# Kernel tuning notes

Hardware: AMD Instinct MI355X
Metric: run time of the kernel (lower is better)

## Reference

```python
import jax, jax.numpy as jnp
import numpy as np

K = 32          # neighbors_for_lrf
EPS = 1e-12     # safe-sqrt epsilon (self-distance is exactly 0)


def shot_lrf(neighborhoods, radii):
    """SHOT local reference frames.
    neighborhoods: (N, K, 3) neighbor offsets (neighbor - center)
    radii:         (N,) support radius (distance to farthest of the K neighbors)
    returns        (N, 3, 3) rows = [x, y, z] axes
    """
    k = neighborhoods.shape[1]
    dists = jnp.sqrt(jnp.maximum(jnp.sum(neighborhoods ** 2, axis=-1), EPS))  # (N,K)
    w = radii[:, None] - dists                                                # (N,K) SHOT weights
    cov = jnp.einsum("nk,nki,nkj->nij", w, neighborhoods, neighborhoods)
    cov = cov / jnp.sum(w, axis=-1)[:, None, None]                            # (N,3,3)

    _, evecs = jnp.linalg.eigh(cov)            # ascending eigenvalues
    x = evecs[:, :, 2]                          # largest-eigenvalue eigenvector
    z = evecs[:, :, 0]                          # smallest-eigenvalue eigenvector

    # Sign disambiguation: orient axis toward the majority of neighbors.
    px = jnp.einsum("nki,ni->nk", neighborhoods, x)
    n_pos_x = jnp.sum(px >= 0, axis=-1)
    x = jnp.where((n_pos_x >= k - n_pos_x)[:, None], x, -x)

    pz = jnp.einsum("nki,ni->nk", neighborhoods, z)
    n_pos_z = jnp.sum(pz >= 0, axis=-1)
    z = jnp.where((n_pos_z >= k - n_pos_z)[:, None], z, -z)

    y = jnp.cross(z, x)
    return jnp.stack([x, y, z], axis=1)         # (N,3,3)


def knn_shot_lrf(k, verts):
    """verts: (N,3) -> (N,3,3) LRFs via KNN + weighted-covariance eigendecomposition."""
    d2 = jnp.sum((verts[:, None, :] - verts[None, :, :]) ** 2, axis=-1)  # (N,N)
    dist = jnp.sqrt(jnp.maximum(d2, EPS))
    neg_top, idx = jax.lax.top_k(-dist, k)      # k nearest (includes self)
    radii = -neg_top[:, -1]                     # distance to farthest kept neighbor
    nbh = verts[idx] - verts[:, None, :]        # (N,K,3) gathered, centered neighborhoods
    return shot_lrf(nbh, radii)


def setup_inputs() -> dict:
    key = jax.random.key(0)
    vertices = jax.random.normal(key, (2, 8192, 3), dtype=jnp.float32)
    return {"vertices": vertices}


def reference(vertices):
    B, N = vertices.shape[0], vertices.shape[1]
    lrfs = jax.vmap(lambda v: knn_shot_lrf(K, v))(vertices)  # (B,N,3,3)
    return lrfs.reshape(B, N, 9)
```

## Files before the change

kernel.cpp:

```cpp
#include <hip/hip_runtime.h>
#include <stdint.h>

#define NPTS 8192
#define KNN  32
#define WAVES 8
#define BTHR (WAVES*64)
#define CAP  512
#define K2BLK 64

#define G     16
#define NCELL 4096
#define TOTC  8192
#define NB    (TOTC/1024)
#define GLO   (-6.0f)
#define GINV  (1.3333334f)

#define EPSF    5.9604645e-08f
#define EPS2F   3.5527137e-15f
#define SAFMINF 1.17549435e-38f
#define SAFMAXF 8.5070592e+37f
#define RTMINF  1.0842022e-19f
#define RTMAXF  9.2233720e+18f

__device__ __forceinline__ float fsignf(float a, float b) {
  return __builtin_copysignf(fabsf(a), b);
}

__device__ __forceinline__ float slapy2f(float x, float y) {
  float xa = fabsf(x), ya = fabsf(y);
  float w = fmaxf(xa, ya), z = fminf(xa, ya);
  if (z == 0.0f) return w;
  float t = __fdiv_rn(z, w);
  return __fmul_rn(w, __fsqrt_rn(__fadd_rn(1.0f, __fmul_rn(t, t))));
}

__device__ __forceinline__ void slartgf(float f, float g, float& c, float& s, float& r) {
  if (g == 0.0f)      { c = 1.0f; s = 0.0f; r = f; }
  else if (f == 0.0f) { c = 0.0f; s = __builtin_copysignf(1.0f, g); r = fabsf(g); }
  else {
    float f1 = fabsf(f), g1 = fabsf(g);
    if (f1 > RTMINF && f1 < RTMAXF && g1 > RTMINF && g1 < RTMAXF) {
      float d = __fsqrt_rn(__fadd_rn(__fmul_rn(f, f), __fmul_rn(g, g)));
      c = __fdiv_rn(f1, d);
      r = __builtin_copysignf(d, f);
      s = __fdiv_rn(g, r);
    } else {
      float u  = fminf(SAFMAXF, fmaxf(SAFMINF, fmaxf(f1, g1)));
      float fs = __fdiv_rn(f, u), gs = __fdiv_rn(g, u);
      float d  = __fsqrt_rn(__fadd_rn(__fmul_rn(fs, fs), __fmul_rn(gs, gs)));
      c = __fdiv_rn(fabsf(fs), d);
      r = __builtin_copysignf(d, f);
      s = __fdiv_rn(gs, r);
      r = __fmul_rn(r, u);
    }
  }
}

__device__ void slaev2f(float a, float b, float c,
                        float& rt1, float& rt2, float& cs1, float& sn1) {
  float sm = __fadd_rn(a, c), df = __fsub_rn(a, c);
  float adf = fabsf(df), tb = __fadd_rn(b, b), ab = fabsf(tb);
  float acmx, acmn;
  if (fabsf(a) > fabsf(c)) { acmx = a; acmn = c; } else { acmx = c; acmn = a; }
  float rt;
  if (adf > ab) {
    float t = __fdiv_rn(ab, adf);
    rt = __fmul_rn(adf, __fsqrt_rn(__fadd_rn(1.0f, __fmul_rn(t, t))));
  } else if (adf < ab) {
    float t = __fdiv_rn(adf, ab);
    rt = __fmul_rn(ab, __fsqrt_rn(__fadd_rn(1.0f, __fmul_rn(t, t))));
  } else {
    rt = __fmul_rn(ab, __fsqrt_rn(2.0f));
  }
  int sgn1;
  if (sm < 0.0f) {
    rt1 = __fmul_rn(0.5f, __fsub_rn(sm, rt)); sgn1 = -1;
    rt2 = __fsub_rn(__fmul_rn(__fdiv_rn(acmx, rt1), acmn), __fmul_rn(__fdiv_rn(b, rt1), b));
  } else if (sm > 0.0f) {
    rt1 = __fmul_rn(0.5f, __fadd_rn(sm, rt)); sgn1 = 1;
    rt2 = __fsub_rn(__fmul_rn(__fdiv_rn(acmx, rt1), acmn), __fmul_rn(__fdiv_rn(b, rt1), b));
  } else {
    rt1 = __fmul_rn(0.5f, rt); rt2 = -rt1; sgn1 = 1;
  }
  float cs; int sgn2;
  if (df >= 0.0f) { cs = __fadd_rn(df, rt); sgn2 = 1; }
  else            { cs = __fsub_rn(df, rt); sgn2 = -1; }
  float acs = fabsf(cs);
  if (acs > ab) {
    float ct = __fdiv_rn(-tb, cs);
    sn1 = __fdiv_rn(1.0f, __fsqrt_rn(__fadd_rn(1.0f, __fmul_rn(ct, ct))));
    cs1 = __fmul_rn(ct, sn1);
  } else {
    if (ab == 0.0f) { cs1 = 1.0f; sn1 = 0.0f; }
    else {
      float tn = __fdiv_rn(-cs, tb);
      cs1 = __fdiv_rn(1.0f, __fsqrt_rn(__fadd_rn(1.0f, __fmul_rn(tn, tn))));
      sn1 = __fmul_rn(tn, cs1);
    }
  }
  if (sgn1 == sgn2) { float tn = cs1; cs1 = -sn1; sn1 = tn; }
}

#define ZZ(i,j) base[((i)*3+(j))*K2BLK]
#define DD(i)   base[(9+(i))*K2BLK]
#define EE(i)   base[(12+(i))*K2BLK]
#define CW(i)   base[(14+(i))*K2BLK]
#define SW(i)   base[(16+(i))*K2BLK]

__device__ void steqr3f(float* base) {
  const int nmaxit = 90;
  int jtot = 0;
  int l1 = 0;
  for (int outer = 0; outer < 6; ++outer) {
    if (l1 > 2) break;
    if (l1 > 0) EE(l1 - 1) = 0.0f;
    int m = 2;
    for (int mm = l1; mm <= 1; ++mm) {
      float tst = fabsf(EE(mm));
      if (tst == 0.0f) { m = mm; break; }
      float thr = __fmul_rn(__fmul_rn(__fsqrt_rn(fabsf(DD(mm))), __fsqrt_rn(fabsf(DD(mm + 1)))), EPSF);
      if (tst <= thr) { EE(mm) = 0.0f; m = mm; break; }
    }
    int l = l1;
    int lend = m;
    l1 = m + 1;
    if (lend == l) continue;
    if (fabsf(DD(lend)) < fabsf(DD(l))) { int t = l; l = lend; lend = t; }
    if (lend > l) {
      for (int it = 0; it < 120; ++it) {
        int m2 = lend;
        if (l != lend) {
          for (int mm = l; mm <= lend - 1; ++mm) {
            float tst = __fmul_rn(EE(mm), EE(mm));
            float thr = __fadd_rn(__fmul_rn(__fmul_rn(EPS2F, fabsf(DD(mm))), fabsf(DD(mm + 1))), SAFMINF);
            if (tst <= thr) { m2 = mm; break; }
          }
        }
        if (m2 < lend) EE(m2) = 0.0f;
        float p = DD(l);
        if (m2 == l) {
          DD(l) = p; l += 1;
          if (l <= lend) continue;
          break;
        }
        if (m2 == l + 1) {
          float rt1, rt2, cc, ss;
          slaev2f(DD(l), EE(l), DD(l + 1), rt1, rt2, cc, ss);
          for (int i = 0; i < 3; ++i) {
            float tz = ZZ(i, l + 1);
            ZZ(i, l + 1) = __fsub_rn(__fmul_rn(cc, tz), __fmul_rn(ss, ZZ(i, l)));
            ZZ(i, l)     = __fadd_rn(__fmul_rn(ss, tz), __fmul_rn(cc, ZZ(i, l)));
          }
          DD(l) = rt1; DD(l + 1) = rt2; EE(l) = 0.0f;
          l += 2;
          if (l <= lend) continue;
          break;
        }
        if (jtot == nmaxit) break;
        jtot++;
        float g = __fdiv_rn(__fsub_rn(DD(l + 1), p), __fmul_rn(2.0f, EE(l)));
        float r = slapy2f(g, 1.0f);
        g = __fadd_rn(__fsub_rn(DD(m2), p), __fdiv_rn(EE(l), __fadd_rn(g, fsignf(r, g))));
        float s = 1.0f, c = 1.0f;
        p = 0.0f;
        for (int i = m2 - 1; i >= l; --i) {
          float f = __fmul_rn(s, EE(i));
          float b = __fmul_rn(c, EE(i));
          slartgf(g, f, c, s, r);
          if (i != m2 - 1) EE(i + 1) = r;
          g = __fsub_rn(DD(i + 1), p);
          r = __fadd_rn(__fmul_rn(__fsub_rn(DD(i), g), s), __fmul_rn(__fmul_rn(2.0f, c), b));
          p = __fmul_rn(s, r);
          DD(i + 1) = __fadd_rn(g, p);
          g = __fsub_rn(__fmul_rn(c, r), b);
          CW(i - l) = c; SW(i - l) = -s;
        }
        int mmc = m2 - l + 1;
        for (int j = mmc - 2; j >= 0; --j) {
          float cj = CW(j), sj = SW(j);
          for (int i = 0; i < 3; ++i) {
            float tz = ZZ(i, l + j + 1);
            ZZ(i, l + j + 1) = __fsub_rn(__fmul_rn(cj, tz), __fmul_rn(sj, ZZ(i, l + j)));
            ZZ(i, l + j)     = __fadd_rn(__fmul_rn(sj, tz), __fmul_rn(cj, ZZ(i, l + j)));
          }
        }
        DD(l) = __fsub_rn(DD(l), p);
        EE(l) = g;
      }
    } else {
      for (int it = 0; it < 120; ++it) {
        int m2 = lend;
        if (l != lend) {
          for (int mm = l; mm >= lend + 1; --mm) {
            float tst = __fmul_rn(EE(mm - 1), EE(mm - 1));
            float thr = __fadd_rn(__fmul_rn(__fmul_rn(EPS2F, fabsf(DD(mm))), fabsf(DD(mm - 1))), SAFMINF);
            if (tst <= thr) { m2 = mm; break; }
          }
        }
        if (m2 > lend) EE(m2 - 1) = 0.0f;
        float p = DD(l);
        if (m2 == l) {
          DD(l) = p; l -= 1;
          if (l >= lend) continue;
          break;
        }
        if (m2 == l - 1) {
          float rt1, rt2, cc, ss;
          slaev2f(DD(l - 1), EE(l - 1), DD(l), rt1, rt2, cc, ss);
          for (int i = 0; i < 3; ++i) {
            float tz = ZZ(i, l);
            ZZ(i, l)     = __fsub_rn(__fmul_rn(cc, tz), __fmul_rn(ss, ZZ(i, l - 1)));
            ZZ(i, l - 1) = __fadd_rn(__fmul_rn(ss, tz), __fmul_rn(cc, ZZ(i, l - 1)));
          }
          DD(l - 1) = rt1; DD(l) = rt2; EE(l - 1) = 0.0f;
          l -= 2;
          if (l >= lend) continue;
          break;
        }
        if (jtot == nmaxit) break;
        jtot++;
        float g = __fdiv_rn(__fsub_rn(DD(l - 1), p), __fmul_rn(2.0f, EE(l - 1)));
        float r = slapy2f(g, 1.0f);
        g = __fadd_rn(__fsub_rn(DD(m2), p), __fdiv_rn(EE(l - 1), __fadd_rn(g, fsignf(r, g))));
        float s = 1.0f, c = 1.0f;
        p = 0.0f;
        for (int i = m2; i <= l - 1; ++i) {
          float f = __fmul_rn(s, EE(i));
          float b = __fmul_rn(c, EE(i));
          slartgf(g, f, c, s, r);
          if (i != m2) EE(i - 1) = r;
          g = __fsub_rn(DD(i), p);
          r = __fadd_rn(__fmul_rn(__fsub_rn(DD(i + 1), g), s), __fmul_rn(__fmul_rn(2.0f, c), b));
          p = __fmul_rn(s, r);
          DD(i) = __fadd_rn(g, p);
          g = __fsub_rn(__fmul_rn(c, r), b);
          CW(i - m2) = c; SW(i - m2) = s;
        }
        int mmc = l - m2 + 1;
        for (int j = 0; j <= mmc - 2; ++j) {
          float cj = CW(j), sj = SW(j);
          for (int i = 0; i < 3; ++i) {
            float tz = ZZ(i, m2 + j + 1);
            ZZ(i, m2 + j + 1) = __fsub_rn(__fmul_rn(cj, tz), __fmul_rn(sj, ZZ(i, m2 + j)));
            ZZ(i, m2 + j)     = __fadd_rn(__fmul_rn(sj, tz), __fmul_rn(cj, ZZ(i, m2 + j)));
          }
        }
        DD(l) = __fsub_rn(DD(l), p);
        EE(l - 1) = g;
      }
    }
    if (jtot >= nmaxit) break;
  }
  for (int ii = 1; ii < 3; ++ii) {
    int i = ii - 1, k = i;
    float p = DD(i);
    for (int j = ii; j < 3; ++j) {
      if (DD(j) < p) { k = j; p = DD(j); }
    }
    if (k != i) {
      DD(k) = DD(i); DD(i) = p;
      for (int r = 0; r < 3; ++r) { float t = ZZ(r, i); ZZ(r, i) = ZZ(r, k); ZZ(r, k) = t; }
    }
  }
}

__device__ __forceinline__ uint32_t d2_ubound(float T) {
  float t2 = __fmul_rn(T, T);
  uint32_t u = __float_as_uint(fmaxf(t2, 0.0f));
  for (int i = 0; i < 64 && u > 0; ++i) {
    if (__fsqrt_rn(fmaxf(__uint_as_float(u), 1e-12f)) <= T) break;
    --u;
  }
  for (int i = 0; i < 64; ++i) {
    if (!(__fsqrt_rn(fmaxf(__uint_as_float(u + 1), 1e-12f)) <= T)) break;
    ++u;
  }
  return u;
}

__device__ __forceinline__ int cellf(float x) {
  int c = (int)floorf(__fmul_rn(__fsub_rn(x, GLO), GINV));
  return c < 0 ? 0 : (c > (G - 1) ? (G - 1) : c);
}


__global__ __launch_bounds__(256)
void hist_kernel(const float* __restrict__ verts, uint32_t* __restrict__ cnt) {
  int i = blockIdx.x * 256 + threadIdx.x;
  const float* p = verts + (size_t)i * 3;
  uint32_t c = (uint32_t)(i >> 13) * (uint32_t)NCELL +
               (((uint32_t)cellf(p[2]) * G + (uint32_t)cellf(p[1])) * G + (uint32_t)cellf(p[0]));
  atomicAdd(&cnt[c], 1u);
}

__global__ __launch_bounds__(1024)
void scanA_kernel(const uint32_t* __restrict__ cnt, uint32_t* __restrict__ start,
                  uint32_t* __restrict__ bsum) {
  __shared__ uint32_t sh[1024];
  int t = threadIdx.x;
  int g = blockIdx.x * 1024 + t;
  uint32_t v = cnt[g];
  sh[t] = v;
  __syncthreads();
  for (int off = 1; off < 1024; off <<= 1) {
    uint32_t u = (t >= off) ? sh[t - off] : 0u;
    __syncthreads();
    sh[t] += u;
    __syncthreads();
  }
  start[g] = sh[t] - v;
  if (t == 1023) bsum[blockIdx.x] = sh[1023];
}

__global__ __launch_bounds__(64)
void scanB_kernel(uint32_t* __restrict__ bsum, uint32_t* __restrict__ start) {
  int lane = threadIdx.x;
  uint32_t v = (lane < NB) ? bsum[lane] : 0u;
  uint32_t inc = v;
  for (int off = 1; off < 64; off <<= 1) {
    uint32_t t = __shfl_up(inc, off);
    if (lane >= off) inc += t;
  }
  if (lane < NB) bsum[lane] = inc - v;
  if (lane == NB - 1) start[TOTC] = inc;
}

__global__ __launch_bounds__(1024)
void scanC_kernel(uint32_t* __restrict__ start, const uint32_t* __restrict__ bsum,
                  uint32_t* __restrict__ cursor) {
  int g = blockIdx.x * 1024 + threadIdx.x;
  start[g] += bsum[blockIdx.x];
  cursor[g] = 0u;
}

__global__ __launch_bounds__(256)
void scatter_kernel(const float* __restrict__ verts, const uint32_t* __restrict__ start,
                    uint32_t* __restrict__ cursor,
                    float* __restrict__ sx, float* __restrict__ sy, float* __restrict__ sz,
                    uint16_t* __restrict__ sidx) {
  int i = blockIdx.x * 256 + threadIdx.x;
  const float* p = verts + (size_t)i * 3;
  float px = p[0], py = p[1], pz = p[2];
  uint32_t c = (uint32_t)(i >> 13) * (uint32_t)NCELL +
               (((uint32_t)cellf(pz) * G + (uint32_t)cellf(py)) * G + (uint32_t)cellf(px));
  uint32_t slot = start[c] + atomicAdd(&cursor[c], 1u);
  sx[slot] = px; sy[slot] = py; sz[slot] = pz;
  sidx[slot] = (uint16_t)(i & (NPTS - 1));
}


__global__ __launch_bounds__(BTHR)
void knn_select_kernel(const float* __restrict__ verts,
                       const uint32_t* __restrict__ cellstart,
                       const float* __restrict__ sx, const float* __restrict__ sy,
                       const float* __restrict__ sz, const uint16_t* __restrict__ sidx,
                       uint16_t* __restrict__ nbr) {
  __shared__ uint64_t SURV[WAVES * CAP];

  const int tid  = threadIdx.x;
  const int w    = tid >> 6;
  const int lane = tid & 63;
  const int query = blockIdx.x * WAVES + w;
  const int b  = query >> 13;
  const int qi = query & (NPTS - 1);
  const float* vb = verts + (size_t)b * NPTS * 3;

  const float qx = vb[3 * qi + 0], qy = vb[3 * qi + 1], qz = vb[3 * qi + 2];

  float sd[4];
#pragma unroll
  for (int s = 0; s < 4; ++s) {
    int j = s * 64 + lane;
    float dxx = __fsub_rn(vb[3 * j + 0], qx);
    float dyy = __fsub_rn(vb[3 * j + 1], qy);
    float dzz = __fsub_rn(vb[3 * j + 2], qz);
    float d2 = __fadd_rn(__fadd_rn(__fmul_rn(dxx, dxx), __fmul_rn(dyy, dyy)), __fmul_rn(dzz, dzz));
    sd[s] = __fsqrt_rn(fmaxf(d2, 1e-12f));
  }
  {
    float lo, hi;
    lo = fminf(sd[0], sd[1]); hi = fmaxf(sd[0], sd[1]); sd[0] = lo; sd[1] = hi;
    lo = fminf(sd[2], sd[3]); hi = fmaxf(sd[2], sd[3]); sd[2] = lo; sd[3] = hi;
    lo = fminf(sd[0], sd[2]); hi = fmaxf(sd[0], sd[2]); sd[0] = lo; sd[2] = hi;
    lo = fminf(sd[1], sd[3]); hi = fmaxf(sd[1], sd[3]); sd[1] = lo; sd[3] = hi;
    lo = fminf(sd[1], sd[2]); hi = fmaxf(sd[1], sd[2]); sd[1] = lo; sd[2] = hi;
  }
  const float INF = __builtin_inff();
  float T = 0.0f;
  for (int r = 0; r < 6; ++r) {
    float g = sd[0];
    for (int o = 32; o; o >>= 1) g = fminf(g, __shfl_xor(g, o));
    bool win = (sd[0] == g) && (g < INF);
    sd[0] = win ? sd[1] : sd[0];
    sd[1] = win ? sd[2] : sd[1];
    sd[2] = win ? sd[3] : sd[2];
    sd[3] = win ? INF   : sd[3];
    if (g < INF) T = g;
  }
  const float Tinit = T;

  const uint64_t lmask_lt = (lane == 0) ? 0ull : (~0ull >> (64 - lane));
  uint32_t U = d2_ubound(T);
  const uint32_t cbase = (uint32_t)b * (uint32_t)NCELL;
  int cnt = 0;
  bool grid_ok = false;
  for (int attempt = 0; attempt < 4; ++attempt) {
    float Tq = __fmul_rn(T, 1.00001f);
    int cx0 = cellf(__fsub_rn(qx, Tq)), cx1 = cellf(__fadd_rn(qx, Tq));
    int cy0 = cellf(__fsub_rn(qy, Tq)), cy1 = cellf(__fadd_rn(qy, Tq));
    int cz0 = cellf(__fsub_rn(qz, Tq)), cz1 = cellf(__fadd_rn(qz, Tq));
    int npairs = (cy1 - cy0 + 1) * (cz1 - cz0 + 1);
    if (npairs > 64) break;
    cnt = 0;
    for (int cz = cz0; cz <= cz1; ++cz) {
      for (int cy = cy0; cy <= cy1; ++cy) {
        uint32_t row = cbase + ((uint32_t)cz * G + (uint32_t)cy) * G;
        uint32_t sbeg = cellstart[row + (uint32_t)cx0];
        uint32_t send = cellstart[row + (uint32_t)cx1 + 1];
        for (uint32_t i0 = sbeg; i0 < send; i0 += 64) {
          uint32_t i = i0 + (uint32_t)lane;
          bool inb = (i < send);
          uint32_t ii = inb ? i : sbeg;
          float dxx = __fsub_rn(sx[ii], qx);
          float dyy = __fsub_rn(sy[ii], qy);
          float dzz = __fsub_rn(sz[ii], qz);
          float d2 = __fadd_rn(__fadd_rn(__fmul_rn(dxx, dxx), __fmul_rn(dyy, dyy)), __fmul_rn(dzz, dzz));
          uint32_t D2 = __float_as_uint(d2);
          bool p = inb && (D2 <= U);
          uint64_t m = __ballot(p);
          if (p) {
            int off = cnt + (int)__popcll(m & lmask_lt);
            if (off < CAP) SURV[w * CAP + off] = ((uint64_t)D2 << 32) | (uint32_t)sidx[ii];
          }
          cnt += (int)__popcll(m);
        }
      }
    }
    if (cnt > CAP)      { T = __fmul_rn(T, 0.7f); U = d2_ubound(T); continue; }
    else if (cnt < KNN) { T = __fmul_rn(T, 1.8f); U = d2_ubound(T); continue; }
    grid_ok = true;
    break;
  }

  bool fast_ok = grid_ok;
  if (!grid_ok) {
    T = Tinit;
    U = d2_ubound(T);
    for (int attempt = 0; attempt < 8; ++attempt) {
      cnt = 0;
#pragma unroll 4
      for (int s = 0; s < NPTS / 64; ++s) {
        int j = s * 64 + lane;
        float dxx = __fsub_rn(vb[3 * j + 0], qx);
        float dyy = __fsub_rn(vb[3 * j + 1], qy);
        float dzz = __fsub_rn(vb[3 * j + 2], qz);
        float d2 = __fadd_rn(__fadd_rn(__fmul_rn(dxx, dxx), __fmul_rn(dyy, dyy)), __fmul_rn(dzz, dzz));
        uint32_t D2 = __float_as_uint(d2);
        bool p = (D2 <= U);
        uint64_t m = __ballot(p);
        if (p) {
          int off = cnt + (int)__popcll(m & lmask_lt);
          if (off < CAP) SURV[w * CAP + off] = ((uint64_t)D2 << 32) | (uint32_t)j;
        }
        cnt += (int)__popcll(m);
      }
      if (cnt > CAP)      { T = __fmul_rn(T, 0.7f); U = d2_ubound(T); continue; }
      else if (cnt < KNN) { T = __fmul_rn(T, 1.8f); U = d2_ubound(T); continue; }
      fast_ok = true;
      break;
    }
  }

  uint32_t myidx = 0xFFFFFFFFu;
  if (fast_ok) {
    const int n = cnt;
    uint64_t kr[8];
#pragma unroll
    for (int t = 0; t < 8; ++t) {
      int idx = lane + (t << 6);
      if (idx < n) {
        uint64_t v = SURV[w * CAP + idx];
        float dist = __fsqrt_rn(fmaxf(__uint_as_float((uint32_t)(v >> 32)), 1e-12f));
        kr[t] = ((uint64_t)__float_as_uint(dist) << 32) | (uint32_t)v;
      } else {
        kr[t] = ~0ull;
      }
    }
    uint64_t last = 0;
    for (int r = 0; r < KNN; ++r) {
      uint64_t lmin = ~0ull;
#pragma unroll
      for (int t = 0; t < 8; ++t) {
        uint64_t v = kr[t];
        if (v > last && v < lmin) lmin = v;
      }
      uint64_t g = lmin;
      for (int o = 32; o; o >>= 1) {
        uint64_t t2 = __shfl_xor((unsigned long long)g, o);
        if (t2 < g) g = t2;
      }
      if (lane == r) myidx = (uint32_t)g;
      last = g;
    }
  } else {
    uint64_t last = 0;
    for (int r = 0; r < KNN; ++r) {
      uint64_t lmin = ~0ull;
      for (int s = 0; s < NPTS / 64; ++s) {
        int j = s * 64 + lane;
        float dxx = __fsub_rn(vb[3 * j + 0], qx);
        float dyy = __fsub_rn(vb[3 * j + 1], qy);
        float dzz = __fsub_rn(vb[3 * j + 2], qz);
        float d2 = __fadd_rn(__fadd_rn(__fmul_rn(dxx, dxx), __fmul_rn(dyy, dyy)), __fmul_rn(dzz, dzz));
        uint64_t key = ((uint64_t)__float_as_uint(__fsqrt_rn(fmaxf(d2, 1e-12f))) << 32) | (uint32_t)j;
        if (key > last && key < lmin) lmin = key;
      }
      uint64_t g = lmin;
      for (int o = 32; o; o >>= 1) {
        uint64_t t2 = __shfl_xor((unsigned long long)g, o);
        if (t2 < g) g = t2;
      }
      if (lane == r) myidx = (uint32_t)g;
      last = g;
    }
  }

  if (lane < KNN) nbr[(size_t)query * KNN + lane] = (uint16_t)myidx;
}


__global__ __launch_bounds__(K2BLK)
void shot_lrf_kernel(const float* __restrict__ verts,
                     const uint16_t* __restrict__ nbr,
                     float* __restrict__ out) {
  __shared__ float EW[18 * K2BLK];

  const int tid = threadIdx.x;
  const int query = blockIdx.x * K2BLK + tid;
  const int b  = query >> 13;
  const int qi = query & (NPTS - 1);
  const float* vb = verts + (size_t)b * NPTS * 3;

  const float qx = vb[3 * qi + 0], qy = vb[3 * qi + 1], qz = vb[3 * qi + 2];

  uint32_t idxs[KNN];
#pragma unroll
  for (int k = 0; k < KNN; ++k)
    idxs[k] = (uint32_t)nbr[(size_t)query * KNN + k] & (NPTS - 1);

  float radii;
  {
    int i31 = (int)idxs[KNN - 1];
    float dxx = __fsub_rn(vb[3 * i31 + 0], qx);
    float dyy = __fsub_rn(vb[3 * i31 + 1], qy);
    float dzz = __fsub_rn(vb[3 * i31 + 2], qz);
    float d2 = __fadd_rn(__fadd_rn(__fmul_rn(dxx, dxx), __fmul_rn(dyy, dyy)), __fmul_rn(dzz, dzz));
    radii = __fsqrt_rn(fmaxf(d2, 1e-12f));
  }

  float rr[8];
#pragma unroll
  for (int i = 0; i < 8; ++i) rr[i] = 0.0f;
  float l00[4], l10[4], l20[4], l11[4], l21[4], l22[4];
#pragma unroll
  for (int L = 0; L < 4; ++L) { l00[L]=0.0f; l10[L]=0.0f; l20[L]=0.0f; l11[L]=0.0f; l21[L]=0.0f; l22[L]=0.0f; }
#pragma unroll
  for (int c = 0; c < 8; ++c) {
#pragma unroll
    for (int L = 0; L < 4; ++L) {
      int k2 = 4 * c + L;
      int idx = (int)idxs[k2];
      float dxx = __fsub_rn(vb[3 * idx + 0], qx);
      float dyy = __fsub_rn(vb[3 * idx + 1], qy);
      float dzz = __fsub_rn(vb[3 * idx + 2], qz);
      float d2 = __fadd_rn(__fadd_rn(__fmul_rn(dxx, dxx), __fmul_rn(dyy, dyy)), __fmul_rn(dzz, dzz));
      float dist = __fsqrt_rn(fmaxf(d2, 1e-12f));
      float wgt = __fsub_rn(radii, dist);
      rr[k2 & 7] = __fadd_rn(rr[k2 & 7], wgt);
      float wx = __fmul_rn(wgt, dxx), wy = __fmul_rn(wgt, dyy), wz = __fmul_rn(wgt, dzz);
      l00[L] = __fadd_rn(l00[L], __fmul_rn(wx, dxx));
      l10[L] = __fadd_rn(l10[L], __fmul_rn(wy, dxx));
      l20[L] = __fadd_rn(l20[L], __fmul_rn(wz, dxx));
      l11[L] = __fadd_rn(l11[L], __fmul_rn(wy, dyy));
      l21[L] = __fadd_rn(l21[L], __fmul_rn(wz, dyy));
      l22[L] = __fadd_rn(l22[L], __fmul_rn(wz, dzz));
    }
  }
  float c00 = __fadd_rn(__fadd_rn(l00[0], l00[1]), __fadd_rn(l00[2], l00[3]));
  float c10 = __fadd_rn(__fadd_rn(l10[0], l10[1]), __fadd_rn(l10[2], l10[3]));
  float c20 = __fadd_rn(__fadd_rn(l20[0], l20[1]), __fadd_rn(l20[2], l20[3]));
  float c11 = __fadd_rn(__fadd_rn(l11[0], l11[1]), __fadd_rn(l11[2], l11[3]));
  float c21 = __fadd_rn(__fadd_rn(l21[0], l21[1]), __fadd_rn(l21[2], l21[3]));
  float c22 = __fadd_rn(__fadd_rn(l22[0], l22[1]), __fadd_rn(l22[2], l22[3]));
  float sumw = __fadd_rn(
      __fadd_rn(__fadd_rn(rr[0], rr[1]), __fadd_rn(rr[2], rr[3])),
      __fadd_rn(__fadd_rn(rr[4], rr[5]), __fadd_rn(rr[6], rr[7])));

  float a11 = __fdiv_rn(c00, sumw);
  float a21 = __fdiv_rn(c10, sumw);
  float a31 = __fdiv_rn(c20, sumw);
  float a22 = __fdiv_rn(c11, sumw);
  float a32 = __fdiv_rn(c21, sumw);
  float a33 = __fdiv_rn(c22, sumw);

  float* base = &EW[tid];
  float taui, v2;
  {
    float alpha = a21;
    float xnorm = fabsf(a31);
    float beta;
    if (xnorm == 0.0f) {
      taui = 0.0f; v2 = 0.0f; beta = alpha;
      DD(0) = a11; DD(1) = a22; DD(2) = a33;
      EE(0) = beta; EE(1) = a32;
    } else {
      beta = -fsignf(slapy2f(alpha, xnorm), alpha);
      taui = __fdiv_rn(__fsub_rn(beta, alpha), beta);
      float inv = __fdiv_rn(1.0f, __fsub_rn(alpha, beta));
      v2 = __fmul_rn(a31, inv);
      float y1 = __fmul_rn(taui, a22);
      float y2 = __fmul_rn(taui, a32);
      float temp2 = __fmul_rn(a32, v2);
      y1 = __fadd_rn(y1, __fmul_rn(taui, temp2));
      y2 = __fadd_rn(y2, __fmul_rn(__fmul_rn(taui, v2), a33));
      float dot = __fadd_rn(y1, __fmul_rn(y2, v2));
      float aw = __fmul_rn(__fmul_rn(-0.5f, taui), dot);
      float w1 = __fadd_rn(y1, aw);
      float w2 = __fadd_rn(y2, __fmul_rn(aw, v2));
      float a22p = __fadd_rn(__fadd_rn(a22, __fmul_rn(1.0f, -w1)), __fmul_rn(w1, -1.0f));
      float a32p = __fadd_rn(__fadd_rn(a32, __fmul_rn(v2, -w1)), __fmul_rn(w2, -1.0f));
      float a33p = __fadd_rn(__fadd_rn(a33, __fmul_rn(v2, -w2)), __fmul_rn(w2, -v2));
      DD(0) = a11; DD(1) = a22p; DD(2) = a33p;
      EE(0) = beta; EE(1) = a32p;
    }
  }

  for (int i = 0; i < 3; ++i)
    for (int j = 0; j < 3; ++j)
      ZZ(i, j) = (i == j) ? 1.0f : 0.0f;

  steqr3f(base);

  if (taui != 0.0f) {
    for (int j = 0; j < 3; ++j) {
      float wj = __fadd_rn(ZZ(1, j), __fmul_rn(ZZ(2, j), v2));
      float t = __fmul_rn(-taui, wj);
      ZZ(1, j) = __fadd_rn(ZZ(1, j), t);
      ZZ(2, j) = __fadd_rn(ZZ(2, j), __fmul_rn(v2, t));
    }
  }

  float X0 = ZZ(0, 2), X1 = ZZ(1, 2), X2 = ZZ(2, 2);
  float Z0 = ZZ(0, 0), Z1 = ZZ(1, 0), Z2 = ZZ(2, 0);

  int npx = 0, npz = 0;
#pragma unroll
  for (int k2 = 0; k2 < KNN; ++k2) {
    int idx = (int)idxs[k2];
    float dxx = __fsub_rn(vb[3 * idx + 0], qx);
    float dyy = __fsub_rn(vb[3 * idx + 1], qy);
    float dzz = __fsub_rn(vb[3 * idx + 2], qz);
    float px = __fadd_rn(__fadd_rn(__fmul_rn(dxx, X0), __fmul_rn(dyy, X1)), __fmul_rn(dzz, X2));
    float pz = __fadd_rn(__fadd_rn(__fmul_rn(dxx, Z0), __fmul_rn(dyy, Z1)), __fmul_rn(dzz, Z2));
    if (px >= 0.0f) npx++;
    if (pz >= 0.0f) npz++;
  }
  if (2 * npx < KNN) { X0 = -X0; X1 = -X1; X2 = -X2; }
  if (2 * npz < KNN) { Z0 = -Z0; Z1 = -Z1; Z2 = -Z2; }

  float Y0 = __fsub_rn(__fmul_rn(Z1, X2), __fmul_rn(Z2, X1));
  float Y1 = __fsub_rn(__fmul_rn(Z2, X0), __fmul_rn(Z0, X2));
  float Y2 = __fsub_rn(__fmul_rn(Z0, X1), __fmul_rn(Z1, X0));

  float* o = out + (size_t)query * 9;
  o[0] = X0; o[1] = X1; o[2] = X2;
  o[3] = Y0; o[4] = Y1; o[5] = Y2;
  o[6] = Z0; o[7] = Z1; o[8] = Z2;
}

#undef ZZ
#undef DD
#undef EE
#undef CW
#undef SW

extern "C" void kernel_launch(void* const* d_in, const int* in_sizes, int n_in,
                              void* d_out, int out_size, void* d_ws, size_t ws_size,
                              hipStream_t stream) {
  (void)n_in; (void)out_size; (void)ws_size;
  const float* verts = (const float*)d_in[0];
  float* out = (float*)d_out;
  int total = in_sizes[0] / 3;

  char* ws = (char*)d_ws;
  uint16_t* nbr    = (uint16_t*)(ws);
  uint32_t* cstart = (uint32_t*)(ws + 1048576);
  uint32_t* ccnt   = (uint32_t*)(ws + 1048576 + 33024);
  uint32_t* bsum   = (uint32_t*)(ws + 1048576 + 33024 + 32768);
  float*    sx     = (float*)   (ws + 1048576 + 33024 + 32768 + 256);
  float*    sy     = sx + 16384;
  float*    sz     = sy + 16384;
  uint16_t* sidx   = (uint16_t*)(sz + 16384);

  hipMemsetAsync(ccnt, 0, (size_t)TOTC * 4, stream);
  hist_kernel   <<<total / 256, 256, 0, stream>>>(verts, ccnt);
  scanA_kernel  <<<NB, 1024, 0, stream>>>(ccnt, cstart, bsum);
  scanB_kernel  <<<1, 64, 0, stream>>>(bsum, cstart);
  scanC_kernel  <<<NB, 1024, 0, stream>>>(cstart, bsum, ccnt);
  scatter_kernel<<<total / 256, 256, 0, stream>>>(verts, cstart, ccnt, sx, sy, sz, sidx);
  knn_select_kernel<<<total / WAVES, BTHR, 0, stream>>>(verts, cstart, sx, sy, sz, sidx, nbr);
  shot_lrf_kernel<<<total / K2BLK, K2BLK, 0, stream>>>(verts, nbr, out);
}
```

Baseline: 187.8 us.

## Merge scan kernels, pack sorted points as float4, prefetch cell ranges per lane

Replaces the three-kernel scan with one single-block scan in which each thread handles 8 cells and also clears the cursors, removing two kernel launches. Sorted points are stored as float4 with the index bit-cast into w, so one vector load replaces four scattered loads in the grid search. Cell row begin/end offsets are loaded in parallel across lanes and broadcast by shuffle instead of being fetched serially, and the top-K selection skips register slots beyond the survivor count. A single-block scan limits parallelism for the prefix sum, and the float4 layout doubles the index storage.

```diff
diff --git a/kernel.cpp b/kernel.cpp
--- a/kernel.cpp
+++ b/kernel.cpp
@@ -11,7 +11,6 @@
 #define G     16
 #define NCELL 4096
 #define TOTC  8192
-#define NB    (TOTC/1024)
 #define GLO   (-6.0f)
 #define GINV  (1.3333334f)
 
@@ -294,13 +293,14 @@
 }
 
 __global__ __launch_bounds__(1024)
-void scanA_kernel(const uint32_t* __restrict__ cnt, uint32_t* __restrict__ start,
-                  uint32_t* __restrict__ bsum) {
+void scan_kernel(uint32_t* __restrict__ cnt, uint32_t* __restrict__ start) {
   __shared__ uint32_t sh[1024];
   int t = threadIdx.x;
-  int g = blockIdx.x * 1024 + t;
-  uint32_t v = cnt[g];
-  sh[t] = v;
+  uint32_t v[8];
+  uint32_t s = 0;
+#pragma unroll
+  for (int k = 0; k < 8; ++k) { v[k] = cnt[t * 8 + k]; s += v[k]; }
+  sh[t] = s;
   __syncthreads();
   for (int off = 1; off < 1024; off <<= 1) {
     uint32_t u = (t >= off) ? sh[t - off] : 0u;
@@ -308,52 +308,32 @@
     sh[t] += u;
     __syncthreads();
   }
-  start[g] = sh[t] - v;
-  if (t == 1023) bsum[blockIdx.x] = sh[1023];
-}
-
-__global__ __launch_bounds__(64)
-void scanB_kernel(uint32_t* __restrict__ bsum, uint32_t* __restrict__ start) {
-  int lane = threadIdx.x;
-  uint32_t v = (lane < NB) ? bsum[lane] : 0u;
-  uint32_t inc = v;
-  for (int off = 1; off < 64; off <<= 1) {
-    uint32_t t = __shfl_up(inc, off);
-    if (lane >= off) inc += t;
-  }
-  if (lane < NB) bsum[lane] = inc - v;
-  if (lane == NB - 1) start[TOTC] = inc;
-}
-
-__global__ __launch_bounds__(1024)
-void scanC_kernel(uint32_t* __restrict__ start, const uint32_t* __restrict__ bsum,
-                  uint32_t* __restrict__ cursor) {
-  int g = blockIdx.x * 1024 + threadIdx.x;
-  start[g] += bsum[blockIdx.x];
-  cursor[g] = 0u;
+  uint32_t run = sh[t] - s;
+#pragma unroll
+  for (int k = 0; k < 8; ++k) { start[t * 8 + k] = run; run += v[k]; cnt[t * 8 + k] = 0u; }
+  if (t == 1023) start[TOTC] = run;
 }
 
 __global__ __launch_bounds__(256)
 void scatter_kernel(const float* __restrict__ verts, const uint32_t* __restrict__ start,
-                    uint32_t* __restrict__ cursor,
-                    float* __restrict__ sx, float* __restrict__ sy, float* __restrict__ sz,
-                    uint16_t* __restrict__ sidx) {
+                    uint32_t* __restrict__ cursor, float4* __restrict__ spts) {
   int i = blockIdx.x * 256 + threadIdx.x;
   const float* p = verts + (size_t)i * 3;
   float px = p[0], py = p[1], pz = p[2];
   uint32_t c = (uint32_t)(i >> 13) * (uint32_t)NCELL +
                (((uint32_t)cellf(pz) * G + (uint32_t)cellf(py)) * G + (uint32_t)cellf(px));
   uint32_t slot = start[c] + atomicAdd(&cursor[c], 1u);
-  sx[slot] = px; sy[slot] = py; sz[slot] = pz;
-  sidx[slot] = (uint16_t)(i & (NPTS - 1));
+  float4 v;
+  v.x = px; v.y = py; v.z = pz;
+  v.w = __uint_as_float((uint32_t)(i & (NPTS - 1)));
+  spts[slot] = v;
 }
 
 
 __global__ __launch_bounds__(BTHR)
 void knn_select_kernel(const float* __restrict__ verts,
                        const uint32_t* __restrict__ cellstart,
-                       const float* __restrict__ sx, const float* __restrict__ sy,
-                       const float* __restrict__ sz, const uint16_t* __restrict__ sidx,
+                       const float4* __restrict__ spts,
                        uint16_t* __restrict__ nbr) {
   __shared__ uint64_t SURV[WAVES * CAP];
 
@@ -409,31 +389,37 @@
     int cx0 = cellf(__fsub_rn(qx, Tq)), cx1 = cellf(__fadd_rn(qx, Tq));
     int cy0 = cellf(__fsub_rn(qy, Tq)), cy1 = cellf(__fadd_rn(qy, Tq));
     int cz0 = cellf(__fsub_rn(qz, Tq)), cz1 = cellf(__fadd_rn(qz, Tq));
-    int npairs = (cy1 - cy0 + 1) * (cz1 - cz0 + 1);
+    int ny = cy1 - cy0 + 1;
+    int npairs = ny * (cz1 - cz0 + 1);
     if (npairs > 64) break;
+    uint32_t sbegv = 0u, sendv = 0u;
+    if (lane < npairs) {
+      int rz = lane / ny, ry = lane - rz * ny;
+      uint32_t row = cbase + ((uint32_t)(cz0 + rz) * G + (uint32_t)(cy0 + ry)) * G;
+      sbegv = cellstart[row + (uint32_t)cx0];
+      sendv = cellstart[row + (uint32_t)cx1 + 1];
+    }
     cnt = 0;
-    for (int cz = cz0; cz <= cz1; ++cz) {
-      for (int cy = cy0; cy <= cy1; ++cy) {
-        uint32_t row = cbase + ((uint32_t)cz * G + (uint32_t)cy) * G;
-        uint32_t sbeg = cellstart[row + (uint32_t)cx0];
-        uint32_t send = cellstart[row + (uint32_t)cx1 + 1];
-        for (uint32_t i0 = sbeg; i0 < send; i0 += 64) {
-          uint32_t i = i0 + (uint32_t)lane;
-          bool inb = (i < send);
-          uint32_t ii = inb ? i : sbeg;
-          float dxx = __fsub_rn(sx[ii], qx);
-          float dyy = __fsub_rn(sy[ii], qy);
-          float dzz = __fsub_rn(sz[ii], qz);
-          float d2 = __fadd_rn(__fadd_rn(__fmul_rn(dxx, dxx), __fmul_rn(dyy, dyy)), __fmul_rn(dzz, dzz));
-          uint32_t D2 = __float_as_uint(d2);
-          bool p = inb && (D2 <= U);
-          uint64_t m = __ballot(p);
-          if (p) {
-            int off = cnt + (int)__popcll(m & lmask_lt);
-            if (off < CAP) SURV[w * CAP + off] = ((uint64_t)D2 << 32) | (uint32_t)sidx[ii];
-          }
-          cnt += (int)__popcll(m);
-        }
+    for (int r = 0; r < npairs; ++r) {
+      uint32_t sbeg = (uint32_t)__shfl((int)sbegv, r);
+      uint32_t send = (uint32_t)__shfl((int)sendv, r);
+      for (uint32_t i0 = sbeg; i0 < send; i0 += 64) {
+        uint32_t i = i0 + (uint32_t)lane;
+        bool inb = (i < send);
+        uint32_t ii = inb ? i : sbeg;
+        float4 v = spts[ii];
+        float dxx = __fsub_rn(v.x, qx);
+        float dyy = __fsub_rn(v.y, qy);
+        float dzz = __fsub_rn(v.z, qz);
+        float d2 = __fadd_rn(__fadd_rn(__fmul_rn(dxx, dxx), __fmul_rn(dyy, dyy)), __fmul_rn(dzz, dzz));
+        uint32_t D2 = __float_as_uint(d2);
+        bool p = inb && (D2 <= U);
+        uint64_t m = __ballot(p);
+        if (p) {
+          int off = cnt + (int)__popcll(m & lmask_lt);
+          if (off < CAP) SURV[w * CAP + off] = ((uint64_t)D2 << 32) | (uint64_t)__float_as_uint(v.w);
+        }
+        cnt += (int)__popcll(m);
       }
     }
     if (cnt > CAP)      { T = __fmul_rn(T, 0.7f); U = d2_ubound(T); continue; }
@@ -491,8 +477,10 @@
       uint64_t lmin = ~0ull;
 #pragma unroll
       for (int t = 0; t < 8; ++t) {
-        uint64_t v = kr[t];
-        if (v > last && v < lmin) lmin = v;
+        if ((t << 6) < n) {
+          uint64_t v = kr[t];
+          if (v > last && v < lmin) lmin = v;
+        }
       }
       uint64_t g = lmin;
       for (int o = 32; o; o >>= 1) {
@@ -696,18 +684,12 @@
   uint16_t* nbr    = (uint16_t*)(ws);
   uint32_t* cstart = (uint32_t*)(ws + 1048576);
   uint32_t* ccnt   = (uint32_t*)(ws + 1048576 + 33024);
-  uint32_t* bsum   = (uint32_t*)(ws + 1048576 + 33024 + 32768);
-  float*    sx     = (float*)   (ws + 1048576 + 33024 + 32768 + 256);
-  float*    sy     = sx + 16384;
-  float*    sz     = sy + 16384;
-  uint16_t* sidx   = (uint16_t*)(sz + 16384);
+  float4*   spts   = (float4*)  (ws + 1048576 + 33024 + 32768);
 
   hipMemsetAsync(ccnt, 0, (size_t)TOTC * 4, stream);
   hist_kernel   <<<total / 256, 256, 0, stream>>>(verts, ccnt);
-  scanA_kernel  <<<NB, 1024, 0, stream>>>(ccnt, cstart, bsum);
-  scanB_kernel  <<<1, 64, 0, stream>>>(bsum, cstart);
-  scanC_kernel  <<<NB, 1024, 0, stream>>>(cstart, bsum, ccnt);
-  scatter_kernel<<<total / 256, 256, 0, stream>>>(verts, cstart, ccnt, sx, sy, sz, sidx);
-  knn_select_kernel<<<total / WAVES, BTHR, 0, stream>>>(verts, cstart, sx, sy, sz, sidx, nbr);
+  scan_kernel   <<<1, 1024, 0, stream>>>(ccnt, cstart);
+  scatter_kernel<<<total / 256, 256, 0, stream>>>(verts, cstart, ccnt, spts);
+  knn_select_kernel<<<total / WAVES, BTHR, 0, stream>>>(verts, cstart, spts, nbr);
   shot_lrf_kernel<<<total / K2BLK, K2BLK, 0, stream>>>(verts, nbr, out);
 }
```

New measurement: 172.6 us, median of 2. 8.1% less time.
